# Optimization experiments

Measured on AMD Instinct MI355X. Metric: run time of the kernel, lower is better.

## Reference

```python
import jax, jax.numpy as jnp
import numpy as np

N = 4096
E = 131072
IN_C, HID, HEADS, OUT_C = 512, 64, 8, 256
BETA = 0.5
NEG_SLOPE = 0.2


def _glorot(key, shape, fan_in, fan_out):
    lim = float(np.sqrt(6.0 / (fan_in + fan_out)))
    return jax.random.uniform(key, shape, jnp.float32, -lim, lim)


def setup_inputs() -> dict:
    key = jax.random.key(0)
    ks = jax.random.split(key, 12)
    x = jax.random.normal(ks[0], (N, IN_C), jnp.float32)
    src = jax.random.randint(ks[1], (E,), 0, N)
    dst = jax.random.randint(ks[2], (E,), 0, N)
    dst = jnp.where(src == dst, (dst + 1) % N, dst)  # no self loops (module removes then re-adds)
    edge_index = jnp.stack([src, dst]).astype(jnp.int64)
    # layer 1: in=512 -> heads=8, out=64 (concat -> 512), residual=False
    W1 = _glorot(ks[3], (IN_C, HEADS * HID), IN_C, HEADS * HID)
    as1 = _glorot(ks[4], (HEADS, HID), HID, HID)
    ad1 = _glorot(ks[5], (HEADS, HID), HID, HID)
    b1 = jnp.zeros((HEADS * HID,), jnp.float32)
    # layer 2: in=512 -> heads=1, out=256, concat=False, residual=True (res_linear needed)
    W2 = _glorot(ks[6], (HEADS * HID, OUT_C), HEADS * HID, OUT_C)
    as2 = _glorot(ks[7], (1, OUT_C), OUT_C, OUT_C)
    ad2 = _glorot(ks[8], (1, OUT_C), OUT_C, OUT_C)
    b2 = jnp.zeros((OUT_C,), jnp.float32)
    resW2 = _glorot(ks[9], (HEADS * HID, OUT_C), HEADS * HID, OUT_C)
    return {"x": x, "edge_index": edge_index, "W1": W1, "as1": as1, "ad1": ad1,
            "b1": b1, "W2": W2, "as2": as2, "ad2": ad2, "b2": b2, "resW2": resW2}


def _seg_softmax(e, seg, n):
    # numerically-stable softmax over edges grouped by destination node
    m = jax.ops.segment_max(e, seg, num_segments=n)  # [n, H]
    a = jnp.exp(e - m[seg])
    s = jax.ops.segment_sum(a, seg, num_segments=n)
    return a / (s[seg] + 1e-16)


def _motif_gat_layer(x, edge_index, W, a_src, a_dst, bias, res_W, heads, out_ch, concat):
    n = x.shape[0]
    residual = x
    h = (x @ W).reshape(n, heads, out_ch)
    # add self loops (input edge_index has none)
    loops = jnp.arange(n, dtype=edge_index.dtype)
    src = jnp.concatenate([edge_index[0], loops])
    dst = jnp.concatenate([edge_index[1], loops])
    xj = h[src]  # [E', H, C]
    xi = h[dst]
    e = (xj * a_src[None]).sum(-1) + (xi * a_dst[None]).sum(-1)  # [E', H]
    alpha_first = _seg_softmax(jax.nn.leaky_relu(e, NEG_SLOPE), dst, n)
    # motif adjacency: dense A^3, row-normalized by clamped row sum
    adj = jnp.zeros((n, n), x.dtype).at[src, dst].set(1.0)
    m3 = adj @ adj @ adj
    m3 = m3 / jnp.clip(m3.sum(-1, keepdims=True), 1.0)
    mw = m3[src, dst][:, None]  # [E', 1]
    alpha_motif = _seg_softmax(jax.nn.leaky_relu(e * mw, NEG_SLOPE), dst, n)
    alpha = BETA * alpha_first + (1.0 - BETA) * alpha_motif  # dropout: eval mode -> identity
    out = jax.ops.segment_sum(alpha[:, :, None] * xj, dst, num_segments=n)  # [n, H, C]
    out = out.reshape(n, heads * out_ch) if concat else out.mean(1)
    if res_W is not None:
        out = out + residual @ res_W
    return out + bias


def reference(x, edge_index, W1, as1, ad1, b1, W2, as2, ad2, b2, resW2):
    h = _motif_gat_layer(x, edge_index, W1, as1, ad1, b1, None, HEADS, HID, True)
    h = jax.nn.elu(h)  # dropout: eval mode -> identity
    out = _motif_gat_layer(h, edge_index, W2, as2, ad2, b2, resW2, 1, OUT_C, False)
    return out
```

## Files before the change

kernel.cpp:

```cpp
#include <hip/hip_runtime.h>
#include <hip/hip_bf16.h>
#include <math.h>

#define NN 4096
#define EE 131072
#define EP (EE + NN)
#define C1 512
#define H1 8
#define C2 256
#define NWORDS 128
#define KP 520

typedef __attribute__((ext_vector_type(8))) short bf16x8;
typedef __attribute__((ext_vector_type(4))) float f32x4;

__device__ __forceinline__ float wredMaxf(float v){
#pragma unroll
  for(int o=32;o;o>>=1) v = fmaxf(v, __shfl_xor(v,o));
  return v;
}
__device__ __forceinline__ float wredSumf(float v){
#pragma unroll
  for(int o=32;o;o>>=1) v += __shfl_xor(v,o);
  return v;
}
__device__ __forceinline__ int wredSumi(int v){
#pragma unroll
  for(int o=32;o;o>>=1) v += __shfl_xor(v,o);
  return v;
}

__device__ __forceinline__ void bfsplit(float v, unsigned short& h, unsigned short& l){
  unsigned bits = __float_as_uint(v);
  h = (unsigned short)(bits>>16);
  float hf = __uint_as_float(bits & 0xFFFF0000u);
  float lo = v - hf;
  l = (unsigned short)(__float_as_uint(lo)>>16);
}

__device__ __forceinline__ unsigned short f2bf_rne(float v){
  unsigned b = __float_as_uint(v);
  return (unsigned short)((b + 0x7FFFu + ((b>>16)&1u)) >> 16);
}

__device__ __forceinline__ int detect_mode(const int* __restrict__ ei32){
  unsigned nz = 0;
#pragma unroll
  for(int i=1;i<16;i+=2) nz |= (unsigned)ei32[i];
  return nz != 0;
}

__device__ __forceinline__ void edge_sd(const int* ei32, int mode, int e, int& s, int& d){
  if(e < EE){
    if(mode==0){ s = ei32[2*e]; d = ei32[2*(EE+e)]; }
    else       { s = ei32[e];   d = ei32[EE+e]; }
  } else { s = e - EE; d = s; }
}

__global__ __launch_bounds__(256) void k_build_cvt(const int* __restrict__ ei32,
    unsigned* __restrict__ rowbits, unsigned* __restrict__ colbits, unsigned* __restrict__ cnt,
    const float* __restrict__ X, unsigned short* __restrict__ xh, unsigned short* __restrict__ xl,
    const float* __restrict__ W1f, const float* __restrict__ W2f, const float* __restrict__ Wrf,
    unsigned short* __restrict__ b1h, unsigned short* __restrict__ b1l,
    unsigned short* __restrict__ b2h, unsigned short* __restrict__ b2l){
  int b = blockIdx.x, t = threadIdx.x;
  if(b < 528){
    int e = b*256 + t;
    if(e >= EP) return;
    int m = detect_mode(ei32), s, d;
    edge_sd(ei32, m, e, s, d);
    atomicOr(&rowbits[s*NWORDS + (d>>5)], 1u<<(d&31));
    atomicOr(&colbits[d*NWORDS + (s>>5)], 1u<<(s&31));
    atomicAdd(&cnt[d], 1u);
  } else if(b < 1552){
    int e = (b-528)*256 + t;
    int row = e >> 6;
    int c0 = (e & 63) * 8;
    const float4 v0 = *(const float4*)&X[(size_t)row*C1 + c0];
    const float4 v1q = *(const float4*)&X[(size_t)row*C1 + c0 + 4];
    float vv[8] = {v0.x,v0.y,v0.z,v0.w,v1q.x,v1q.y,v1q.z,v1q.w};
    unsigned short h[8], l[8];
#pragma unroll
    for(int j=0;j<8;j++) bfsplit(vv[j], h[j], l[j]);
    *(bf16x8*)&xh[(size_t)row*KP + c0] = *(bf16x8*)h;
    *(bf16x8*)&xl[(size_t)row*KP + c0] = *(bf16x8*)l;
  } else {
    int blk = b - 1552;
    const float* W; int N, n, nrow; unsigned short *bh, *bl;
    if(blk < 512){ W=W1f; N=512; n=blk;     nrow=n;     bh=b1h; bl=b1l; }
    else if(blk < 768){ W=W2f; N=256; n=blk-512; nrow=n;     bh=b2h; bl=b2l; }
    else { W=Wrf; N=256; n=blk-768; nrow=n+256; bh=b2h; bl=b2l; }
    int k = t*2;
    float a = W[(size_t)k*N + n];
    float bb = W[(size_t)(k+1)*N + n];
    unsigned short h0,l0,h1,l1;
    bfsplit(a,h0,l0); bfsplit(bb,h1,l1);
    unsigned short hp[2]={h0,h1}, lp[2]={l0,l1};
    *(unsigned int*)&bh[(size_t)nrow*KP + k] = *(unsigned int*)hp;
    *(unsigned int*)&bl[(size_t)nrow*KP + k] = *(unsigned int*)lp;
  }
}

__global__ __launch_bounds__(256) void k_scan_deg(const unsigned* __restrict__ cnt, unsigned* __restrict__ rowptr,
    const unsigned* __restrict__ rowbits, float* __restrict__ v1){
  int t = threadIdx.x;
  if(blockIdx.x == 0){
    __shared__ unsigned part[256];
    unsigned loc[16]; unsigned s = 0;
#pragma unroll
    for(int i=0;i<16;i++){ loc[i]=cnt[t*16+i]; s+=loc[i]; }
    part[t]=s; __syncthreads();
    for(int off=1;off<256;off<<=1){
      unsigned v = (t>=off)? part[t-off] : 0u;
      __syncthreads();
      part[t]+=v;
      __syncthreads();
    }
    unsigned run = (t==0)? 0u : part[t-1];
#pragma unroll
    for(int i=0;i<16;i++){ rowptr[t*16+i]=run; run+=loc[i]; }
    if(t==255) rowptr[NN]=run;
  } else {
    int node = (blockIdx.x-1)*4 + (t>>6);
    int lane = t & 63;
    unsigned w0 = rowbits[node*NWORDS + 2*lane];
    unsigned w1 = rowbits[node*NWORDS + 2*lane + 1];
    int c = __popc(w0) + __popc(w1);
    c = wredSumi(c);
    if(lane==0) v1[node] = (float)c;
  }
}

__global__ __launch_bounds__(256) void k_fill_mv(const int* __restrict__ ei32,
    const unsigned* __restrict__ rowptr, unsigned* __restrict__ fill, unsigned* __restrict__ csr_src,
    const unsigned* __restrict__ rowbits, const float* __restrict__ v1, float* __restrict__ v2){
  int t = threadIdx.x;
  if(blockIdx.x < 528){
    int e = blockIdx.x*256 + t;
    if(e >= EP) return;
    int m = detect_mode(ei32), s, d;
    edge_sd(ei32, m, e, s, d);
    unsigned pos = rowptr[d] + atomicAdd(&fill[d], 1u);
    csr_src[pos]=(unsigned)s;
  } else {
    int node = (blockIdx.x-528)*4 + (t>>6);
    int lane = t & 63;
    float sum = 0.f;
    unsigned w = rowbits[node*NWORDS + 2*lane]; int b0 = lane*64;
    while(w){ int b=__ffs(w)-1; sum += v1[b0+b]; w &= w-1; }
    w = rowbits[node*NWORDS + 2*lane + 1]; b0 = lane*64 + 32;
    while(w){ int b=__ffs(w)-1; sum += v1[b0+b]; w &= w-1; }
    sum = wredSumf(sum);
    if(lane==0) v2[node] = sum;
  }
}

__global__ __launch_bounds__(256) void k_mv2(const unsigned* __restrict__ rowbits,
    const float* __restrict__ v2, float* __restrict__ v3){
  int node = blockIdx.x*4 + (threadIdx.x>>6);
  int lane = threadIdx.x & 63;
  float sum = 0.f;
  unsigned w = rowbits[node*NWORDS + 2*lane]; int b0 = lane*64;
  while(w){ int b=__ffs(w)-1; sum += v2[b0+b]; w &= w-1; }
  w = rowbits[node*NWORDS + 2*lane + 1]; b0 = lane*64 + 32;
  while(w){ int b=__ffs(w)-1; sum += v2[b0+b]; w &= w-1; }
  sum = wredSumf(sum);
  if(lane==0) v3[node] = sum;
}

__device__ __forceinline__ void gemm_tile(unsigned short* lds, int bx, int by,
    const unsigned short* __restrict__ Ah, const unsigned short* __restrict__ Al,
    const unsigned short* __restrict__ Bh, const unsigned short* __restrict__ Bl,
    unsigned short* __restrict__ Cb, float* __restrict__ resf,
    const float* __restrict__ aS, const float* __restrict__ aD,
    float* __restrict__ oS, float* __restrict__ oD, int amode){
  unsigned short* Ahs = lds;
  unsigned short* Als = lds + 64*72;
  unsigned short* Bhs = lds + 2*64*72;
  unsigned short* Bls = lds + 3*64*72;
  int bm = by*64, bn = bx*64;
  int t = threadIdx.x, lane = t&63, w = t>>6;
  int wm = (w>>1)*32, wn = (w&1)*32;
  f32x4 acc[2][2];
#pragma unroll
  for(int i=0;i<2;i++)
#pragma unroll
    for(int j=0;j<2;j++) acc[i][j] = (f32x4){0.f,0.f,0.f,0.f};
  int sm = t>>2, sk = (t&3)*16;
  const unsigned short* pAh = &Ah[(size_t)(bm+sm)*KP + sk];
  const unsigned short* pAl = &Al[(size_t)(bm+sm)*KP + sk];
  const unsigned short* pBh = &Bh[(size_t)(bn+sm)*KP + sk];
  const unsigned short* pBl = &Bl[(size_t)(bn+sm)*KP + sk];
  int fr = lane&15, kg = lane>>4;
  bf16x8 rah0 = *(const bf16x8*)(pAh), rah1 = *(const bf16x8*)(pAh+8);
  bf16x8 ral0 = *(const bf16x8*)(pAl), ral1 = *(const bf16x8*)(pAl+8);
  bf16x8 rbh0 = *(const bf16x8*)(pBh), rbh1 = *(const bf16x8*)(pBh+8);
  bf16x8 rbl0 = *(const bf16x8*)(pBl), rbl1 = *(const bf16x8*)(pBl+8);
  *(bf16x8*)&Ahs[sm*72+sk] = rah0; *(bf16x8*)&Ahs[sm*72+sk+8] = rah1;
  *(bf16x8*)&Als[sm*72+sk] = ral0; *(bf16x8*)&Als[sm*72+sk+8] = ral1;
  *(bf16x8*)&Bhs[sm*72+sk] = rbh0; *(bf16x8*)&Bhs[sm*72+sk+8] = rbh1;
  *(bf16x8*)&Bls[sm*72+sk] = rbl0; *(bf16x8*)&Bls[sm*72+sk+8] = rbl1;
  __syncthreads();
  for(int k0=0;k0<C1;k0+=64){
    int kn = k0+64;
    if(kn<C1){
      rah0 = *(const bf16x8*)(pAh+kn); rah1 = *(const bf16x8*)(pAh+kn+8);
      ral0 = *(const bf16x8*)(pAl+kn); ral1 = *(const bf16x8*)(pAl+kn+8);
      rbh0 = *(const bf16x8*)(pBh+kn); rbh1 = *(const bf16x8*)(pBh+kn+8);
      rbl0 = *(const bf16x8*)(pBl+kn); rbl1 = *(const bf16x8*)(pBl+kn+8);
    }
#pragma unroll
    for(int ks=0;ks<64;ks+=32){
      bf16x8 fah[2], fal[2], fbh[2], fbl[2];
#pragma unroll
      for(int i=0;i<2;i++){
        fah[i] = *(bf16x8*)&Ahs[(wm + i*16 + fr)*72 + ks + kg*8];
        fal[i] = *(bf16x8*)&Als[(wm + i*16 + fr)*72 + ks + kg*8];
        fbh[i] = *(bf16x8*)&Bhs[(wn + i*16 + fr)*72 + ks + kg*8];
        fbl[i] = *(bf16x8*)&Bls[(wn + i*16 + fr)*72 + ks + kg*8];
      }
#pragma unroll
      for(int i=0;i<2;i++)
#pragma unroll
        for(int j=0;j<2;j++){
          acc[i][j] = __builtin_amdgcn_mfma_f32_16x16x32_bf16(fah[i], fbh[j], acc[i][j], 0,0,0);
          acc[i][j] = __builtin_amdgcn_mfma_f32_16x16x32_bf16(fah[i], fbl[j], acc[i][j], 0,0,0);
          acc[i][j] = __builtin_amdgcn_mfma_f32_16x16x32_bf16(fal[i], fbh[j], acc[i][j], 0,0,0);
        }
    }
    __syncthreads();
    if(kn<C1){
      *(bf16x8*)&Ahs[sm*72+sk] = rah0; *(bf16x8*)&Ahs[sm*72+sk+8] = rah1;
      *(bf16x8*)&Als[sm*72+sk] = ral0; *(bf16x8*)&Als[sm*72+sk+8] = ral1;
      *(bf16x8*)&Bhs[sm*72+sk] = rbh0; *(bf16x8*)&Bhs[sm*72+sk+8] = rbh1;
      *(bf16x8*)&Bls[sm*72+sk] = rbl0; *(bf16x8*)&Bls[sm*72+sk+8] = rbl1;
    }
    __syncthreads();
  }
#pragma unroll
  for(int i=0;i<2;i++)
#pragma unroll
    for(int j=0;j<2;j++){
      int gr = bm + wm + i*16 + kg*4;
      int gc = bn + wn + j*16 + fr;
      if(amode==1){
#pragma unroll
        for(int e=0;e<4;e++)
          Cb[(size_t)(gr+e)*C1 + gc] = f2bf_rne(acc[i][j][e]);
      } else {
        if(gc < 256){
#pragma unroll
          for(int e=0;e<4;e++)
            Cb[(size_t)(gr+e)*C2 + gc] = f2bf_rne(acc[i][j][e]);
        } else {
#pragma unroll
          for(int e=0;e<4;e++)
            resf[(size_t)(gr+e)*C2 + gc - 256] = acc[i][j][e];
        }
      }
    }
  bool do_attn = (amode==1) || (bn < 256);
  if(do_attn){
    float p1[2][4], p2[2][4];
#pragma unroll
    for(int i=0;i<2;i++)
#pragma unroll
      for(int e=0;e<4;e++){ p1[i][e]=0.f; p2[i][e]=0.f; }
#pragma unroll
    for(int j=0;j<2;j++){
      int col = bn + wn + j*16 + fr;
      float a1c = aS[col], a2c = aD[col];
#pragma unroll
      for(int i=0;i<2;i++)
#pragma unroll
        for(int e=0;e<4;e++){ p1[i][e] += acc[i][j][e]*a1c; p2[i][e] += acc[i][j][e]*a2c; }
    }
#pragma unroll
    for(int o=1;o<16;o<<=1){
#pragma unroll
      for(int i=0;i<2;i++)
#pragma unroll
        for(int e=0;e<4;e++){ p1[i][e]+=__shfl_xor(p1[i][e],o); p2[i][e]+=__shfl_xor(p2[i][e],o); }
    }
    if(fr==0){
      int head = (amode==1)? (bn>>6) : 0;
      int hs = (amode==1)? H1 : 1;
#pragma unroll
      for(int i=0;i<2;i++)
#pragma unroll
        for(int e=0;e<4;e++){
          int row = bm + wm + i*16 + kg*4 + e;
          atomicAdd(&oS[row*hs + head], p1[i][e]);
          atomicAdd(&oD[row*hs + head], p2[i][e]);
        }
    }
  }
}

__device__ __forceinline__ void unswizzle_g(int b, int& bx, int& by){
  by = (b&7) + ((b>>6)<<3);
  bx = (b>>3)&7;
}

__global__ __launch_bounds__(256) void k_gemm1_motif(
    const unsigned short* __restrict__ Ah, const unsigned short* __restrict__ Al,
    const unsigned short* __restrict__ Bh, const unsigned short* __restrict__ Bl,
    unsigned short* __restrict__ hpreb, const float* __restrict__ as1, const float* __restrict__ ad1,
    float* __restrict__ asrc1, float* __restrict__ adst1,
    const unsigned* __restrict__ rowbits, const unsigned* __restrict__ colbits,
    const unsigned* __restrict__ rowptr, const unsigned* __restrict__ csr_src,
    const float* __restrict__ v3, float* __restrict__ mwc){
  __shared__ union {
    unsigned short g[4*64*72];
    struct { unsigned short nbr[4][192]; int cntL[4]; } m;
  } sm;
  int b = blockIdx.x, t = threadIdx.x;
  if(b < 512){
    int bx, by; unswizzle_g(b, bx, by);
    gemm_tile(sm.g, bx, by, Ah, Al, Bh, Bl, hpreb, nullptr,
              as1, ad1, asrc1, adst1, 1);
    return;
  }
  int lane = t&63, wv = t>>6;
  int d = (b-512)*4 + wv;
  if(lane==0) sm.m.cntL[wv]=0;
  {
    unsigned w = colbits[d*NWORDS + 2*lane]; int b0 = lane*64;
    while(w){ int bb=__ffs(w)-1; int pos=atomicAdd(&sm.m.cntL[wv],1); sm.m.nbr[wv][pos]=(unsigned short)(b0+bb); w&=w-1; }
    w = colbits[d*NWORDS + 2*lane + 1]; b0 = lane*64 + 32;
    while(w){ int bb=__ffs(w)-1; int pos=atomicAdd(&sm.m.cntL[wv],1); sm.m.nbr[wv][pos]=(unsigned short)(b0+bb); w&=w-1; }
  }
  __syncthreads();
  int m = sm.m.cntL[wv];
  unsigned gp[8][2];
#pragma unroll
  for(int p=0;p<8;p++){ gp[p][0]=0u; gp[p][1]=0u; }
  for(int t0=0;t0<m;t0+=8){
    unsigned xa[8], xb[8];
#pragma unroll
    for(int j=0;j<8;j++){
      int tt=t0+j;
      if(tt<m){ int l = sm.m.nbr[wv][tt]; xa[j]=colbits[l*NWORDS+2*lane]; xb[j]=colbits[l*NWORDS+2*lane+1]; }
      else    { xa[j]=0u; xb[j]=0u; }
    }
#pragma unroll
    for(int j=0;j<8;j++){
      unsigned c = xa[j];
#pragma unroll
      for(int p=0;p<8;p++){ unsigned cy = gp[p][0] & c; gp[p][0] ^= c; c = cy; }
      c = xb[j];
#pragma unroll
      for(int p=0;p<8;p++){ unsigned cy = gp[p][1] & c; gp[p][1] ^= c; c = cy; }
    }
  }
  unsigned base = rowptr[d], deg = rowptr[d+1]-base;
  for(unsigned i0=0;i0<deg;i0+=8){
    unsigned sidx[8], ra[8], rb[8];
#pragma unroll
    for(int j=0;j<8;j++){
      unsigned ii = (i0+j < deg) ? (i0+j) : (deg-1);
      sidx[j] = csr_src[base+ii];
    }
#pragma unroll
    for(int j=0;j<8;j++){ ra[j]=rowbits[sidx[j]*NWORDS+2*lane]; rb[j]=rowbits[sidx[j]*NWORDS+2*lane+1]; }
    int sum[8];
#pragma unroll
    for(int j=0;j<8;j++){
      int s=0;
#pragma unroll
      for(int p=0;p<8;p++)
        s += (__popc(ra[j]&gp[p][0]) + __popc(rb[j]&gp[p][1])) << p;
      sum[j]=s;
    }
    int pk[4];
#pragma unroll
    for(int j=0;j<4;j++) pk[j] = sum[2*j] | (sum[2*j+1]<<16);
#pragma unroll
    for(int j=0;j<4;j++) pk[j] = wredSumi(pk[j]);
    if(lane==0){
#pragma unroll
      for(int j=0;j<8;j++){
        unsigned idx = i0+j;
        if(idx<deg){
          int ss = (j&1)? ((pk[j>>1]>>16)&0xFFFF) : (pk[j>>1]&0xFFFF);
          mwc[base+idx] = (float)ss / fmaxf(v3[csr_src[base+idx]], 1.0f);
        }
      }
    }
  }
}

__global__ __launch_bounds__(256) void k_gemm2(
    const unsigned short* __restrict__ Ah, const unsigned short* __restrict__ Al,
    const unsigned short* __restrict__ Bh, const unsigned short* __restrict__ Bl,
    unsigned short* __restrict__ h2b, float* __restrict__ resf,
    const float* __restrict__ as2, const float* __restrict__ ad2,
    float* __restrict__ asrc2, float* __restrict__ adst2){
  __shared__ unsigned short lds[4*64*72];
  int bx, by; unswizzle_g(blockIdx.x, bx, by);
  gemm_tile(lds, bx, by, Ah, Al, Bh, Bl, h2b, resf,
            as2, ad2, asrc2, adst2, 2);
}

__global__ __launch_bounds__(128) void k_layer1(const unsigned* __restrict__ rowptr, const unsigned* __restrict__ csr_src,
    const float* __restrict__ mwc, const float* __restrict__ asrc, const float* __restrict__ adst,
    const unsigned short* __restrict__ hpreb, const float* __restrict__ b1,
    unsigned short* __restrict__ h1h, unsigned short* __restrict__ h1l){
  int n = blockIdx.x;
  int tid = threadIdx.x, lane = tid&63, wv = tid>>6;
  unsigned base = rowptr[n], deg = rowptr[n+1]-base;
  __shared__ float a1s[128][9];
  __shared__ float a2s[128][9];
  __shared__ unsigned ssrc[128];
  __shared__ float red1[2][8], red2[2][8];
  __shared__ float snm1[8], snm2[8], sscl1[8], sscl2[8];
  __shared__ float sS1[8], sS2[8], sM1[8], sM2[8];
  __shared__ float adsts[8];
  if(tid<8){ adsts[tid]=adst[n*H1+tid]; sM1[tid]=-3.0e38f; sM2[tid]=-3.0e38f; sS1[tid]=0.f; sS2[tid]=0.f; }
  __syncthreads();
  int h = tid>>4;
  float4 acc1={0.f,0.f,0.f,0.f}, acc2={0.f,0.f,0.f,0.f};
  for(unsigned c0=0;c0<deg;c0+=128){
    int csz = (int)min(128u, deg-c0);
    bool act = (tid < csz);
    float el[8], em[8];
    if(act){
      unsigned s = csr_src[base+c0+tid];
      ssrc[tid]=s;
      float mwv = mwc[base+c0+tid];
      const float4 a0v = *(const float4*)&asrc[s*H1];
      const float4 a1v = *(const float4*)&asrc[s*H1+4];
      float as8[8]={a0v.x,a0v.y,a0v.z,a0v.w,a1v.x,a1v.y,a1v.z,a1v.w};
#pragma unroll
      for(int hh=0;hh<8;hh++){
        float ev = as8[hh]+adsts[hh];
        el[hh] = ev>=0.f? ev : 0.2f*ev;
        float evm = ev*mwv;
        em[hh] = evm>=0.f? evm : 0.2f*evm;
      }
    } else {
#pragma unroll
      for(int hh=0;hh<8;hh++){ el[hh]=-3.0e38f; em[hh]=-3.0e38f; }
    }
    float mx1[8], mx2[8];
#pragma unroll
    for(int hh=0;hh<8;hh++){ mx1[hh]=wredMaxf(el[hh]); mx2[hh]=wredMaxf(em[hh]); }
    if(lane==0){
#pragma unroll
      for(int hh=0;hh<8;hh++){ red1[wv][hh]=mx1[hh]; red2[wv][hh]=mx2[hh]; }
    }
    __syncthreads();
    if(tid<8){
      float cm1 = fmaxf(red1[0][tid], red1[1][tid]);
      float cm2 = fmaxf(red2[0][tid], red2[1][tid]);
      float nm1 = fmaxf(sM1[tid], cm1), nm2 = fmaxf(sM2[tid], cm2);
      sscl1[tid] = expf(sM1[tid]-nm1); sscl2[tid] = expf(sM2[tid]-nm2);
      snm1[tid]=nm1; snm2[tid]=nm2;
      sM1[tid]=nm1;  sM2[tid]=nm2;
    }
    __syncthreads();
    float s1l[8], s2l[8];
#pragma unroll
    for(int hh=0;hh<8;hh++){
      float a1v = act? expf(el[hh]-snm1[hh]) : 0.f;
      float a2v = act? expf(em[hh]-snm2[hh]) : 0.f;
      if(act){ a1s[tid][hh]=a1v; a2s[tid][hh]=a2v; }
      s1l[hh]=a1v; s2l[hh]=a2v;
    }
#pragma unroll
    for(int hh=0;hh<8;hh++){ s1l[hh]=wredSumf(s1l[hh]); s2l[hh]=wredSumf(s2l[hh]); }
    if(lane==0){
#pragma unroll
      for(int hh=0;hh<8;hh++){ red1[wv][hh]=s1l[hh]; red2[wv][hh]=s2l[hh]; }
    }
    __syncthreads();
    if(tid<8){
      sS1[tid] = sS1[tid]*sscl1[tid] + red1[0][tid]+red1[1][tid];
      sS2[tid] = sS2[tid]*sscl2[tid] + red2[0][tid]+red2[1][tid];
    }
    {
      float sc1 = sscl1[h], sc2 = sscl2[h];
      acc1.x*=sc1; acc1.y*=sc1; acc1.z*=sc1; acc1.w*=sc1;
      acc2.x*=sc2; acc2.y*=sc2; acc2.z*=sc2; acc2.w*=sc2;
    }
    for(int i0=0;i0<csz;i0+=8){
      int jn = min(8, csz-i0);
      unsigned sj[8]; float a1j[8], a2j[8];
#pragma unroll
      for(int j=0;j<8;j++){
        int ii = (j<jn)? i0+j : i0;
        sj[j]=ssrc[ii]; a1j[j]=a1s[ii][h]; a2j[j]=a2s[ii][h];
      }
      ushort4 hq[8];
#pragma unroll
      for(int j=0;j<8;j++) hq[j] = *(const ushort4*)&hpreb[(size_t)sj[j]*C1 + tid*4];
#pragma unroll
      for(int j=0;j<8;j++){
        float w1 = (j<jn)? a1j[j] : 0.f;
        float w2 = (j<jn)? a2j[j] : 0.f;
        float hx = __uint_as_float((unsigned)hq[j].x<<16);
        float hy = __uint_as_float((unsigned)hq[j].y<<16);
        float hz = __uint_as_float((unsigned)hq[j].z<<16);
        float hw = __uint_as_float((unsigned)hq[j].w<<16);
        acc1.x += w1*hx; acc1.y += w1*hy; acc1.z += w1*hz; acc1.w += w1*hw;
        acc2.x += w2*hx; acc2.y += w2*hy; acc2.z += w2*hz; acc2.w += w2*hw;
      }
    }
    __syncthreads();
  }
  float r1 = 0.5f/(sS1[h]+1e-16f), r2 = 0.5f/(sS2[h]+1e-16f);
  int cc = tid*4;
  const float4 bv = *(const float4*)&b1[cc];
  float o[4];
  float vx = acc1.x*r1 + acc2.x*r2 + bv.x; o[0] = vx>0.f? vx : expm1f(vx);
  float vy = acc1.y*r1 + acc2.y*r2 + bv.y; o[1] = vy>0.f? vy : expm1f(vy);
  float vz = acc1.z*r1 + acc2.z*r2 + bv.z; o[2] = vz>0.f? vz : expm1f(vz);
  float vw = acc1.w*r1 + acc2.w*r2 + bv.w; o[3] = vw>0.f? vw : expm1f(vw);
  unsigned short hh4[4], ll4[4];
#pragma unroll
  for(int j=0;j<4;j++) bfsplit(o[j], hh4[j], ll4[j]);
  *(ushort4*)&h1h[(size_t)n*KP + cc] = *(ushort4*)hh4;
  *(ushort4*)&h1l[(size_t)n*KP + cc] = *(ushort4*)ll4;
}

__global__ __launch_bounds__(64) void k_layer2(const unsigned* __restrict__ rowptr, const unsigned* __restrict__ csr_src,
    const float* __restrict__ mwc, const float* __restrict__ asrc, const float* __restrict__ adst,
    const unsigned short* __restrict__ h2b, const float* __restrict__ res,
    const float* __restrict__ b2, float* __restrict__ out){
  int n = blockIdx.x; int lane = threadIdx.x;
  unsigned base = rowptr[n], deg = rowptr[n+1]-base;
  __shared__ float a1s[64], a2s[64];
  __shared__ unsigned ssrc[64];
  float ad = adst[n];
  float M1=-3.0e38f, M2=-3.0e38f, S1=0.f, S2=0.f;
  float4 acc1={0.f,0.f,0.f,0.f}, acc2={0.f,0.f,0.f,0.f};
  for(unsigned c0=0;c0<deg;c0+=64){
    int csz = (int)min(64u, deg-c0);
    bool act = (lane < csz);
    float el=-3.0e38f, em=-3.0e38f;
    if(act){
      unsigned s = csr_src[base+c0+lane];
      ssrc[lane]=s;
      float mwv = mwc[base+c0+lane];
      float ev = asrc[s] + ad;
      el = ev>=0.f? ev : 0.2f*ev;
      float evm = ev*mwv;
      em = evm>=0.f? evm : 0.2f*evm;
    }
    float nm1 = fmaxf(M1, wredMaxf(el));
    float nm2 = fmaxf(M2, wredMaxf(em));
    float sc1 = expf(M1-nm1), sc2 = expf(M2-nm2);
    M1=nm1; M2=nm2;
    float a1 = act? expf(el-nm1) : 0.f;
    float a2 = act? expf(em-nm2) : 0.f;
    if(act){ a1s[lane]=a1; a2s[lane]=a2; }
    S1 = S1*sc1 + wredSumf(a1);
    S2 = S2*sc2 + wredSumf(a2);
    acc1.x*=sc1; acc1.y*=sc1; acc1.z*=sc1; acc1.w*=sc1;
    acc2.x*=sc2; acc2.y*=sc2; acc2.z*=sc2; acc2.w*=sc2;
    __syncthreads();
    for(int i0=0;i0<csz;i0+=8){
      int jn = min(8, csz-i0);
      unsigned sj[8]; float a1j[8], a2j[8];
#pragma unroll
      for(int j=0;j<8;j++){
        int ii = (j<jn)? i0+j : i0;
        sj[j]=ssrc[ii]; a1j[j]=a1s[ii]; a2j[j]=a2s[ii];
      }
      ushort4 hq[8];
#pragma unroll
      for(int j=0;j<8;j++) hq[j] = *(const ushort4*)&h2b[(size_t)sj[j]*C2 + lane*4];
#pragma unroll
      for(int j=0;j<8;j++){
        float w1 = (j<jn)? a1j[j] : 0.f;
        float w2 = (j<jn)? a2j[j] : 0.f;
        float hx = __uint_as_float((unsigned)hq[j].x<<16);
        float hy = __uint_as_float((unsigned)hq[j].y<<16);
        float hz = __uint_as_float((unsigned)hq[j].z<<16);
        float hw = __uint_as_float((unsigned)hq[j].w<<16);
        acc1.x += w1*hx; acc1.y += w1*hy; acc1.z += w1*hz; acc1.w += w1*hw;
        acc2.x += w2*hx; acc2.y += w2*hy; acc2.z += w2*hz; acc2.w += w2*hw;
      }
    }
    __syncthreads();
  }
  float r1 = 0.5f/(S1+1e-16f), r2 = 0.5f/(S2+1e-16f);
  int cc = lane*4;
  const float4 rv = *(const float4*)&res[(size_t)n*C2 + cc];
  const float4 bv = *(const float4*)&b2[cc];
  float4 o = {acc1.x*r1 + acc2.x*r2 + rv.x + bv.x,
              acc1.y*r1 + acc2.y*r2 + rv.y + bv.y,
              acc1.z*r1 + acc2.z*r2 + rv.z + bv.z,
              acc1.w*r1 + acc2.w*r2 + rv.w + bv.w};
  *(float4*)&out[(size_t)n*C2 + cc] = o;
}

extern "C" void kernel_launch(void* const* d_in, const int* in_sizes, int n_in,
                              void* d_out, int out_size, void* d_ws, size_t ws_size,
                              hipStream_t stream) {
  const float* x    = (const float*)d_in[0];
  const int*   ei32 = (const int*)d_in[1];
  const float* W1   = (const float*)d_in[2];
  const float* as1  = (const float*)d_in[3];
  const float* ad1  = (const float*)d_in[4];
  const float* b1   = (const float*)d_in[5];
  const float* W2   = (const float*)d_in[6];
  const float* as2  = (const float*)d_in[7];
  const float* ad2  = (const float*)d_in[8];
  const float* b2   = (const float*)d_in[9];
  const float* resW2= (const float*)d_in[10];
  float* out = (float*)d_out;

  char* p = (char*)d_ws;
  auto alloc = [&](size_t b){ void* r=(void*)p; p += (b + 255) & ~(size_t)255; return r; };
  unsigned* rowbits = (unsigned*)alloc((size_t)NN*NWORDS*4);
  unsigned* colbits = (unsigned*)alloc((size_t)NN*NWORDS*4);
  unsigned* cnt     = (unsigned*)alloc(NN*4);
  unsigned* fill    = (unsigned*)alloc(NN*4);
  float* asrc1= (float*)alloc(NN*H1*4);
  float* adst1= (float*)alloc(NN*H1*4);
  float* asrc2= (float*)alloc(NN*4);
  float* adst2= (float*)alloc(NN*4);
  size_t zbytes = (size_t)(p - (char*)rowbits);
  unsigned* rowptr  = (unsigned*)alloc((NN+4)*4);
  float* v1 = (float*)alloc(NN*4);
  float* v2 = (float*)alloc(NN*4);
  float* v3 = (float*)alloc(NN*4);
  unsigned* csr_src = (unsigned*)alloc((size_t)EP*4);
  float* mwc  = (float*)alloc((size_t)EP*4);
  unsigned short* xsh = (unsigned short*)alloc((size_t)NN*KP*2);
  unsigned short* xsl = (unsigned short*)alloc((size_t)NN*KP*2);
  unsigned short* bt1h= (unsigned short*)alloc((size_t)C1*KP*2);
  unsigned short* bt1l= (unsigned short*)alloc((size_t)C1*KP*2);
  unsigned short* bt2h= (unsigned short*)alloc((size_t)C1*KP*2);
  unsigned short* bt2l= (unsigned short*)alloc((size_t)C1*KP*2);
  unsigned short* hpreb = (unsigned short*)alloc((size_t)NN*C1*2);
  unsigned short* h1h = (unsigned short*)alloc((size_t)NN*KP*2);
  unsigned short* h1l = (unsigned short*)alloc((size_t)NN*KP*2);
  unsigned short* h2b = (unsigned short*)alloc((size_t)NN*C2*2);
  float* res  = (float*)alloc((size_t)NN*C2*4);

  hipMemsetAsync(rowbits, 0, zbytes, stream);

  k_build_cvt<<<2576,256,0,stream>>>(ei32, rowbits, colbits, cnt,
                                     x, xsh, xsl, W1, W2, resW2, bt1h, bt1l, bt2h, bt2l);
  k_scan_deg<<<1+NN/4,256,0,stream>>>(cnt, rowptr, rowbits, v1);
  k_fill_mv<<<528+NN/4,256,0,stream>>>(ei32, rowptr, fill, csr_src, rowbits, v1, v2);
  k_mv2<<<NN/4,256,0,stream>>>(rowbits, v2, v3);

  k_gemm1_motif<<<512+NN/4,256,0,stream>>>(xsh, xsl, bt1h, bt1l, hpreb, as1, ad1, asrc1, adst1,
                                           rowbits, colbits, rowptr, csr_src, v3, mwc);
  k_layer1<<<NN,128,0,stream>>>(rowptr, csr_src, mwc, asrc1, adst1, hpreb, b1, h1h, h1l);

  k_gemm2<<<512,256,0,stream>>>(h1h, h1l, bt2h, bt2l, h2b, res, as2, ad2, asrc2, adst2);
  k_layer2<<<NN,64,0,stream>>>(rowptr, csr_src, mwc, asrc2, adst2, h2b, res, b2, out);
}
```

Measured before the change: 241.1 us.

## Load GEMM MFMA fragments directly from global memory, dropping LDS staging

Rewrites the split-bf16 GEMM tile so each wave loads its MFMA operand fragments straight from global memory, in a fully unrolled 16-step K loop, instead of staging 64x64 tiles through LDS with double-buffered registers and two barriers per step. This removes the LDS traffic and __syncthreads, and shrinks shared memory use in both GEMM kernels and the fused motif kernel, which may raise occupancy. The cost is redundant global/L2 reads, since each A and B fragment is now fetched by two waves, and there is no explicit prefetch to hide load latency.

```diff
diff --git a/kernel.cpp b/kernel.cpp
--- a/kernel.cpp
+++ b/kernel.cpp
@@ -168,74 +168,52 @@
   if(lane==0) v3[node] = sum;
 }
 
-__device__ __forceinline__ void gemm_tile(unsigned short* lds, int bx, int by,
+__device__ __forceinline__ void gemm_tile(int bx, int by,
     const unsigned short* __restrict__ Ah, const unsigned short* __restrict__ Al,
     const unsigned short* __restrict__ Bh, const unsigned short* __restrict__ Bl,
     unsigned short* __restrict__ Cb, float* __restrict__ resf,
     const float* __restrict__ aS, const float* __restrict__ aD,
     float* __restrict__ oS, float* __restrict__ oD, int amode){
-  unsigned short* Ahs = lds;
-  unsigned short* Als = lds + 64*72;
-  unsigned short* Bhs = lds + 2*64*72;
-  unsigned short* Bls = lds + 3*64*72;
   int bm = by*64, bn = bx*64;
   int t = threadIdx.x, lane = t&63, w = t>>6;
   int wm = (w>>1)*32, wn = (w&1)*32;
+  int fr = lane&15, kg = lane>>4;
   f32x4 acc[2][2];
 #pragma unroll
   for(int i=0;i<2;i++)
 #pragma unroll
     for(int j=0;j<2;j++) acc[i][j] = (f32x4){0.f,0.f,0.f,0.f};
-  int sm = t>>2, sk = (t&3)*16;
-  const unsigned short* pAh = &Ah[(size_t)(bm+sm)*KP + sk];
-  const unsigned short* pAl = &Al[(size_t)(bm+sm)*KP + sk];
-  const unsigned short* pBh = &Bh[(size_t)(bn+sm)*KP + sk];
-  const unsigned short* pBl = &Bl[(size_t)(bn+sm)*KP + sk];
-  int fr = lane&15, kg = lane>>4;
-  bf16x8 rah0 = *(const bf16x8*)(pAh), rah1 = *(const bf16x8*)(pAh+8);
-  bf16x8 ral0 = *(const bf16x8*)(pAl), ral1 = *(const bf16x8*)(pAl+8);
-  bf16x8 rbh0 = *(const bf16x8*)(pBh), rbh1 = *(const bf16x8*)(pBh+8);
-  bf16x8 rbl0 = *(const bf16x8*)(pBl), rbl1 = *(const bf16x8*)(pBl+8);
-  *(bf16x8*)&Ahs[sm*72+sk] = rah0; *(bf16x8*)&Ahs[sm*72+sk+8] = rah1;
-  *(bf16x8*)&Als[sm*72+sk] = ral0; *(bf16x8*)&Als[sm*72+sk+8] = ral1;
-  *(bf16x8*)&Bhs[sm*72+sk] = rbh0; *(bf16x8*)&Bhs[sm*72+sk+8] = rbh1;
-  *(bf16x8*)&Bls[sm*72+sk] = rbl0; *(bf16x8*)&Bls[sm*72+sk+8] = rbl1;
-  __syncthreads();
-  for(int k0=0;k0<C1;k0+=64){
-    int kn = k0+64;
-    if(kn<C1){
-      rah0 = *(const bf16x8*)(pAh+kn); rah1 = *(const bf16x8*)(pAh+kn+8);
-      ral0 = *(const bf16x8*)(pAl+kn); ral1 = *(const bf16x8*)(pAl+kn+8);
-      rbh0 = *(const bf16x8*)(pBh+kn); rbh1 = *(const bf16x8*)(pBh+kn+8);
-      rbl0 = *(const bf16x8*)(pBl+kn); rbl1 = *(const bf16x8*)(pBl+kn+8);
-    }
-#pragma unroll
-    for(int ks=0;ks<64;ks+=32){
-      bf16x8 fah[2], fal[2], fbh[2], fbl[2];
-#pragma unroll
-      for(int i=0;i<2;i++){
-        fah[i] = *(bf16x8*)&Ahs[(wm + i*16 + fr)*72 + ks + kg*8];
-        fal[i] = *(bf16x8*)&Als[(wm + i*16 + fr)*72 + ks + kg*8];
-        fbh[i] = *(bf16x8*)&Bhs[(wn + i*16 + fr)*72 + ks + kg*8];
-        fbl[i] = *(bf16x8*)&Bls[(wn + i*16 + fr)*72 + ks + kg*8];
-      }
-#pragma unroll
-      for(int i=0;i<2;i++)
-#pragma unroll
-        for(int j=0;j<2;j++){
-          acc[i][j] = __builtin_amdgcn_mfma_f32_16x16x32_bf16(fah[i], fbh[j], acc[i][j], 0,0,0);
-          acc[i][j] = __builtin_amdgcn_mfma_f32_16x16x32_bf16(fah[i], fbl[j], acc[i][j], 0,0,0);
-          acc[i][j] = __builtin_amdgcn_mfma_f32_16x16x32_bf16(fal[i], fbh[j], acc[i][j], 0,0,0);
-        }
-    }
-    __syncthreads();
-    if(kn<C1){
-      *(bf16x8*)&Ahs[sm*72+sk] = rah0; *(bf16x8*)&Ahs[sm*72+sk+8] = rah1;
-      *(bf16x8*)&Als[sm*72+sk] = ral0; *(bf16x8*)&Als[sm*72+sk+8] = ral1;
-      *(bf16x8*)&Bhs[sm*72+sk] = rbh0; *(bf16x8*)&Bhs[sm*72+sk+8] = rbh1;
-      *(bf16x8*)&Bls[sm*72+sk] = rbl0; *(bf16x8*)&Bls[sm*72+sk+8] = rbl1;
-    }
-    __syncthreads();
+  const unsigned short* pAh0 = &Ah[(size_t)(bm+wm+fr)*KP + kg*8];
+  const unsigned short* pAh1 = pAh0 + (size_t)16*KP;
+  const unsigned short* pAl0 = &Al[(size_t)(bm+wm+fr)*KP + kg*8];
+  const unsigned short* pAl1 = pAl0 + (size_t)16*KP;
+  const unsigned short* pBh0 = &Bh[(size_t)(bn+wn+fr)*KP + kg*8];
+  const unsigned short* pBh1 = pBh0 + (size_t)16*KP;
+  const unsigned short* pBl0 = &Bl[(size_t)(bn+wn+fr)*KP + kg*8];
+  const unsigned short* pBl1 = pBl0 + (size_t)16*KP;
+#pragma unroll
+  for(int c=0;c<16;c++){
+    int k0 = c*32;
+    bf16x8 ah0 = *(const bf16x8*)(pAh0 + k0);
+    bf16x8 ah1 = *(const bf16x8*)(pAh1 + k0);
+    bf16x8 al0 = *(const bf16x8*)(pAl0 + k0);
+    bf16x8 al1 = *(const bf16x8*)(pAl1 + k0);
+    bf16x8 bh0 = *(const bf16x8*)(pBh0 + k0);
+    bf16x8 bh1 = *(const bf16x8*)(pBh1 + k0);
+    bf16x8 bl0 = *(const bf16x8*)(pBl0 + k0);
+    bf16x8 bl1 = *(const bf16x8*)(pBl1 + k0);
+    acc[0][0] = __builtin_amdgcn_mfma_f32_16x16x32_bf16(ah0, bh0, acc[0][0], 0,0,0);
+    acc[0][1] = __builtin_amdgcn_mfma_f32_16x16x32_bf16(ah0, bh1, acc[0][1], 0,0,0);
+    acc[1][0] = __builtin_amdgcn_mfma_f32_16x16x32_bf16(ah1, bh0, acc[1][0], 0,0,0);
+    acc[1][1] = __builtin_amdgcn_mfma_f32_16x16x32_bf16(ah1, bh1, acc[1][1], 0,0,0);
+    acc[0][0] = __builtin_amdgcn_mfma_f32_16x16x32_bf16(ah0, bl0, acc[0][0], 0,0,0);
+    acc[0][1] = __builtin_amdgcn_mfma_f32_16x16x32_bf16(ah0, bl1, acc[0][1], 0,0,0);
+    acc[1][0] = __builtin_amdgcn_mfma_f32_16x16x32_bf16(ah1, bl0, acc[1][0], 0,0,0);
+    acc[1][1] = __builtin_amdgcn_mfma_f32_16x16x32_bf16(ah1, bl1, acc[1][1], 0,0,0);
+    acc[0][0] = __builtin_amdgcn_mfma_f32_16x16x32_bf16(al0, bh0, acc[0][0], 0,0,0);
+    acc[0][1] = __builtin_amdgcn_mfma_f32_16x16x32_bf16(al0, bh1, acc[0][1], 0,0,0);
+    acc[1][0] = __builtin_amdgcn_mfma_f32_16x16x32_bf16(al1, bh0, acc[1][0], 0,0,0);
+    acc[1][1] = __builtin_amdgcn_mfma_f32_16x16x32_bf16(al1, bh1, acc[1][1], 0,0,0);
   }
 #pragma unroll
   for(int i=0;i<2;i++)
@@ -310,28 +288,26 @@
     const unsigned* __restrict__ rowbits, const unsigned* __restrict__ colbits,
     const unsigned* __restrict__ rowptr, const unsigned* __restrict__ csr_src,
     const float* __restrict__ v3, float* __restrict__ mwc){
-  __shared__ union {
-    unsigned short g[4*64*72];
-    struct { unsigned short nbr[4][192]; int cntL[4]; } m;
-  } sm;
+  __shared__ unsigned short nbr_s[4][192];
+  __shared__ int cntL_s[4];
   int b = blockIdx.x, t = threadIdx.x;
   if(b < 512){
     int bx, by; unswizzle_g(b, bx, by);
-    gemm_tile(sm.g, bx, by, Ah, Al, Bh, Bl, hpreb, nullptr,
+    gemm_tile(bx, by, Ah, Al, Bh, Bl, hpreb, nullptr,
               as1, ad1, asrc1, adst1, 1);
     return;
   }
   int lane = t&63, wv = t>>6;
   int d = (b-512)*4 + wv;
-  if(lane==0) sm.m.cntL[wv]=0;
+  if(lane==0) cntL_s[wv]=0;
   {
     unsigned w = colbits[d*NWORDS + 2*lane]; int b0 = lane*64;
-    while(w){ int bb=__ffs(w)-1; int pos=atomicAdd(&sm.m.cntL[wv],1); sm.m.nbr[wv][pos]=(unsigned short)(b0+bb); w&=w-1; }
+    while(w){ int bb=__ffs(w)-1; int pos=atomicAdd(&cntL_s[wv],1); nbr_s[wv][pos]=(unsigned short)(b0+bb); w&=w-1; }
     w = colbits[d*NWORDS + 2*lane + 1]; b0 = lane*64 + 32;
-    while(w){ int bb=__ffs(w)-1; int pos=atomicAdd(&sm.m.cntL[wv],1); sm.m.nbr[wv][pos]=(unsigned short)(b0+bb); w&=w-1; }
+    while(w){ int bb=__ffs(w)-1; int pos=atomicAdd(&cntL_s[wv],1); nbr_s[wv][pos]=(unsigned short)(b0+bb); w&=w-1; }
   }
   __syncthreads();
-  int m = sm.m.cntL[wv];
+  int m = cntL_s[wv];
   unsigned gp[8][2];
 #pragma unroll
   for(int p=0;p<8;p++){ gp[p][0]=0u; gp[p][1]=0u; }
@@ -340,7 +316,7 @@
 #pragma unroll
     for(int j=0;j<8;j++){
       int tt=t0+j;
-      if(tt<m){ int l = sm.m.nbr[wv][tt]; xa[j]=colbits[l*NWORDS+2*lane]; xb[j]=colbits[l*NWORDS+2*lane+1]; }
+      if(tt<m){ int l = nbr_s[wv][tt]; xa[j]=colbits[l*NWORDS+2*lane]; xb[j]=colbits[l*NWORDS+2*lane+1]; }
       else    { xa[j]=0u; xb[j]=0u; }
     }
 #pragma unroll
@@ -396,9 +372,8 @@
     unsigned short* __restrict__ h2b, float* __restrict__ resf,
     const float* __restrict__ as2, const float* __restrict__ ad2,
     float* __restrict__ asrc2, float* __restrict__ adst2){
-  __shared__ unsigned short lds[4*64*72];
   int bx, by; unswizzle_g(blockIdx.x, bx, by);
-  gemm_tile(lds, bx, by, Ah, Al, Bh, Bl, h2b, resf,
+  gemm_tile(bx, by, Ah, Al, Bh, Bl, h2b, resf,
             as2, ad2, asrc2, adst2, 2);
 }
 
```

Result: slower. 248.4 us (+3.0%).
